# Kernel optimization log

Measured on AMD Instinct MI355X. Metric: run time of the kernel, lower is better.

The kernel has to match this reference:

```python
import jax, jax.numpy as jnp
import numpy as np
import math

E = 1024
H = 16
R = 16
ALPHA = 16
SCALING = ALPHA / R
T, B, S = 2048, 2, 2048


def setup_inputs() -> dict:
    key = jax.random.key(0)
    ks = jax.random.split(key, 20)
    d = {
        "query": jax.random.normal(ks[0], (T, B, E), jnp.float32),
        "key": jax.random.normal(ks[1], (S, B, E), jnp.float32),
        "value": jax.random.normal(ks[2], (S, B, E), jnp.float32),
    }
    i = 3
    for name in ("q", "k", "v", "o"):
        d[name + "_w"] = jax.random.normal(ks[i], (E, E), jnp.float32) * 0.02; i += 1
        d[name + "_b"] = jax.random.normal(ks[i], (E,), jnp.float32) * 0.02; i += 1
        d[name + "_la"] = jax.random.normal(ks[i], (R, E), jnp.float32) * 0.02; i += 1
        d[name + "_lb"] = jax.random.normal(ks[i], (E, R), jnp.float32) * 0.02; i += 1
    return d


def _lora_linear(x, w, b, la, lb):
    # y = x @ w.T + b + scaling * (x @ la.T) @ lb.T
    return x @ w.T + b + SCALING * ((x @ la.T) @ lb.T)


def reference(query, key, value,
              q_w, q_b, q_la, q_lb,
              k_w, k_b, k_la, k_lb,
              v_w, v_b, v_la, v_lb,
              o_w, o_b, o_la, o_lb):
    tgt_len, bsz, embed_dim = query.shape
    src_len = key.shape[0]
    head_dim = embed_dim // H
    q = _lora_linear(query, q_w, q_b, q_la, q_lb)
    k = _lora_linear(key, k_w, k_b, k_la, k_lb)
    v = _lora_linear(value, v_w, v_b, v_la, v_lb)
    # (T, B, E) -> (B*H, T, hd)
    q = q.reshape(tgt_len, bsz * H, head_dim).transpose(1, 0, 2)
    k = k.reshape(src_len, bsz * H, head_dim).transpose(1, 0, 2)
    v = v.reshape(src_len, bsz * H, head_dim).transpose(1, 0, 2)
    scale = 1.0 / math.sqrt(float(head_dim))
    scores = jnp.einsum("btd,bsd->bts", q * scale, k)  # (B*H, T, S)
    attn = jax.nn.softmax(scores, axis=-1)
    out = jnp.einsum("bts,bsd->btd", attn, v)  # (B*H, T, hd)
    out = out.transpose(1, 0, 2).reshape(tgt_len * bsz, embed_dim)
    out = _lora_linear(out, o_w, o_b, o_la, o_lb)
    out = out.reshape(tgt_len, bsz, embed_dim)
    attn_w = attn.reshape(bsz, H, tgt_len, src_len).mean(axis=1)
    return out, attn_w
```

## Files before the change

kernel.cpp:

```cpp
#include <hip/hip_runtime.h>
#include <stdint.h>

#define E_DIM 1024
#define KAUG 1056
#define N_HEADS 16
#define HD 64
#define R_LORA 16
#define T_LEN 2048
#define B_SZ 2
#define S_LEN 2048
#define NROW 4096
#define Q_SCALE 0.1803368801111204f

#define XG_N ((size_t)NROW * KAUG)
#define WG_N ((size_t)E_DIM * KAUG)
#define HSZ  ((size_t)B_SZ * N_HEADS * T_LEN * HD)

typedef unsigned short USH;
typedef __bf16 bf16x8 __attribute__((ext_vector_type(8)));
typedef float  f32x4  __attribute__((ext_vector_type(4)));

__device__ __forceinline__ USH f2bf(float f) {
    uint32_t u = __builtin_bit_cast(uint32_t, f);
    return (USH)((u + 0x7FFFu + ((u >> 16) & 1u)) >> 16);
}
__device__ __forceinline__ float bf2f(USH s) {
    uint32_t u = ((uint32_t)s) << 16;
    return __builtin_bit_cast(float, u);
}
__device__ __forceinline__ void async_cp16(const void* g, void* l) {
    __builtin_amdgcn_global_load_lds(
        (const __attribute__((address_space(1))) void*)g,
        (__attribute__((address_space(3))) void*)l, 16, 0, 0);
}
__device__ __forceinline__ uint32_t pack_bf_trunc(float x, float y) {
    return __builtin_amdgcn_perm(__builtin_bit_cast(uint32_t, y),
                                 __builtin_bit_cast(uint32_t, x), 0x07060302u);
}

__global__ __launch_bounds__(256) void lora_aug_x3_kernel(
    const float* __restrict__ Xq, const float* __restrict__ Xk,
    const float* __restrict__ Xv,
    const float* __restrict__ laq, const float* __restrict__ lak,
    const float* __restrict__ lav, USH* __restrict__ Xg_base) {
    int n = blockIdx.x, y = blockIdx.y, tid = threadIdx.x;
    const float* X  = (y == 0) ? Xq : (y == 1) ? Xk : Xv;
    const float* la = (y == 0) ? laq : (y == 1) ? lak : lav;
    USH* Xg = Xg_base + (size_t)y * XG_N;

    float4 xv = *(const float4*)(X + (size_t)n * E_DIM + tid * 4);
    ushort4 ox;
    ox.x = f2bf(xv.x); ox.y = f2bf(xv.y); ox.z = f2bf(xv.z); ox.w = f2bf(xv.w);
    *(ushort4*)(Xg + (size_t)n * KAUG + tid * 4) = ox;

    float acc[R_LORA];
#pragma unroll
    for (int r = 0; r < R_LORA; ++r) {
        float4 lv = *(const float4*)(la + (size_t)r * E_DIM + tid * 4);
        acc[r] = xv.x * lv.x + xv.y * lv.y + xv.z * lv.z + xv.w * lv.w;
    }
#pragma unroll
    for (int r = 0; r < R_LORA; ++r) {
        float v = acc[r];
#pragma unroll
        for (int off = 32; off > 0; off >>= 1) v += __shfl_down(v, off, 64);
        acc[r] = v;
    }
    __shared__ float red[R_LORA][4];
    int lane = tid & 63, wid = tid >> 6;
    if (lane == 0) {
#pragma unroll
        for (int r = 0; r < R_LORA; ++r) red[r][wid] = acc[r];
    }
    __syncthreads();
    if (tid < 32) {
        float v = 0.0f;
        if (tid < R_LORA) v = red[tid][0] + red[tid][1] + red[tid][2] + red[tid][3];
        else if (tid == R_LORA) v = 1.0f;
        Xg[(size_t)n * KAUG + 1024 + tid] = f2bf(v);
    }
}

__global__ __launch_bounds__(256) void lora_a_bf16_kernel(
    USH* __restrict__ Xg, const float* __restrict__ la) {
    int n = blockIdx.x, tid = threadIdx.x;
    ushort4 xu = *(const ushort4*)(Xg + (size_t)n * KAUG + tid * 4);
    float x0 = bf2f(xu.x), x1 = bf2f(xu.y), x2 = bf2f(xu.z), x3 = bf2f(xu.w);
    float acc[R_LORA];
#pragma unroll
    for (int r = 0; r < R_LORA; ++r) {
        float4 lv = *(const float4*)(la + (size_t)r * E_DIM + tid * 4);
        acc[r] = x0 * lv.x + x1 * lv.y + x2 * lv.z + x3 * lv.w;
    }
#pragma unroll
    for (int r = 0; r < R_LORA; ++r) {
        float v = acc[r];
#pragma unroll
        for (int off = 32; off > 0; off >>= 1) v += __shfl_down(v, off, 64);
        acc[r] = v;
    }
    __shared__ float red[R_LORA][4];
    int lane = tid & 63, wid = tid >> 6;
    if (lane == 0) {
#pragma unroll
        for (int r = 0; r < R_LORA; ++r) red[r][wid] = acc[r];
    }
    __syncthreads();
    if (tid < 32) {
        float v = 0.0f;
        if (tid < R_LORA) v = red[tid][0] + red[tid][1] + red[tid][2] + red[tid][3];
        else if (tid == R_LORA) v = 1.0f;
        Xg[(size_t)n * KAUG + 1024 + tid] = f2bf(v);
    }
}

__global__ __launch_bounds__(256) void aug_w4_kernel(
    const float* __restrict__ Wq, const float* __restrict__ lbq, const float* __restrict__ bq,
    const float* __restrict__ Wk, const float* __restrict__ lbk, const float* __restrict__ bk_,
    const float* __restrict__ Wv, const float* __restrict__ lbv, const float* __restrict__ bv_,
    const float* __restrict__ Wo, const float* __restrict__ lbo, const float* __restrict__ bo,
    USH* __restrict__ Wg_base) {
    int e = blockIdx.x, y = blockIdx.y, tid = threadIdx.x;
    const float* W    = (y == 0) ? Wq : (y == 1) ? Wk : (y == 2) ? Wv : Wo;
    const float* lb   = (y == 0) ? lbq : (y == 1) ? lbk : (y == 2) ? lbv : lbo;
    const float* bias = (y == 0) ? bq : (y == 1) ? bk_ : (y == 2) ? bv_ : bo;
    USH* Wg = Wg_base + (size_t)y * WG_N;

    float4 v = *(const float4*)(W + (size_t)e * E_DIM + tid * 4);
    ushort4 o;
    o.x = f2bf(v.x); o.y = f2bf(v.y); o.z = f2bf(v.z); o.w = f2bf(v.w);
    *(ushort4*)(Wg + (size_t)e * KAUG + tid * 4) = o;
    if (tid < 32) {
        float t = (tid < R_LORA) ? lb[(size_t)e * R_LORA + tid]
                                 : (tid == R_LORA ? bias[e] : 0.0f);
        Wg[(size_t)e * KAUG + 1024 + tid] = f2bf(t);
    }
}

__global__ __launch_bounds__(256) void gemm_qkv_kernel(
    const USH* __restrict__ Xg_base, const USH* __restrict__ Wg_base,
    USH* __restrict__ qkv_base) {
    __shared__ __align__(16) USH As[2][128 * 32];
    __shared__ __align__(16) USH Bs[2][128 * 32];

    int orig = blockIdx.x + (blockIdx.y << 3) + blockIdx.z * 256;
    int v_ = (orig & 7) * 96 + (orig >> 3);
    int e0 = (v_ & 7) * 128, n0 = ((v_ >> 3) & 31) * 128, z = v_ >> 8;

    const USH* Xg = Xg_base + (size_t)z * XG_N;
    const USH* Wg = Wg_base + (size_t)z * WG_N;
    USH* out = qkv_base + (size_t)z * HSZ;
    float scale = (z == 0) ? Q_SCALE : 1.0f;

    int tid = threadIdx.x;
    int wid = tid >> 6, lane = tid & 63, quad = lane >> 4, l16 = lane & 15;
    int wm = wid & 1, wn = wid >> 1;

    int r0 = wid * 16 + (lane >> 2);
    int k8 = (lane & 3) * 8;

    f32x4 acc[4][4];
    const f32x4 fzero = {0.f, 0.f, 0.f, 0.f};
#pragma unroll
    for (int i = 0; i < 4; ++i)
#pragma unroll
        for (int j = 0; j < 4; ++j) acc[i][j] = fzero;

    async_cp16(Xg + (size_t)(n0 + r0) * KAUG + k8,       As[0] + (wid * 16) * 32);
    async_cp16(Xg + (size_t)(n0 + 64 + r0) * KAUG + k8,  As[0] + (64 + wid * 16) * 32);
    async_cp16(Wg + (size_t)(e0 + r0) * KAUG + k8,       Bs[0] + (wid * 16) * 32);
    async_cp16(Wg + (size_t)(e0 + 64 + r0) * KAUG + k8,  Bs[0] + (64 + wid * 16) * 32);
    __syncthreads();

    int cur = 0;
    for (int kt = 0; kt < KAUG; kt += 32, cur ^= 1) {
        if (kt + 32 < KAUG) {
            int kn = kt + 32;
            async_cp16(Xg + (size_t)(n0 + r0) * KAUG + kn + k8,       As[cur ^ 1] + (wid * 16) * 32);
            async_cp16(Xg + (size_t)(n0 + 64 + r0) * KAUG + kn + k8,  As[cur ^ 1] + (64 + wid * 16) * 32);
            async_cp16(Wg + (size_t)(e0 + r0) * KAUG + kn + k8,       Bs[cur ^ 1] + (wid * 16) * 32);
            async_cp16(Wg + (size_t)(e0 + 64 + r0) * KAUG + kn + k8,  Bs[cur ^ 1] + (64 + wid * 16) * 32);
        }

        bf16x8 af[4], bfr[4];
#pragma unroll
        for (int i = 0; i < 4; ++i)
            af[i] = *(const bf16x8*)&As[cur][(wm * 64 + i * 16 + l16) * 32 + quad * 8];
#pragma unroll
        for (int j = 0; j < 4; ++j)
            bfr[j] = *(const bf16x8*)&Bs[cur][(wn * 64 + j * 16 + l16) * 32 + quad * 8];
#pragma unroll
        for (int i = 0; i < 4; ++i)
#pragma unroll
            for (int j = 0; j < 4; ++j)
                acc[i][j] = __builtin_amdgcn_mfma_f32_16x16x32_bf16(
                    af[i], bfr[j], acc[i][j], 0, 0, 0);

        __syncthreads();
    }

#pragma unroll
    for (int i = 0; i < 4; ++i) {
#pragma unroll
        for (int j = 0; j < 4; ++j) {
#pragma unroll
            for (int r = 0; r < 4; ++r) {
                int nr = n0 + wm * 64 + i * 16 + quad * 4 + r;
                int ec = e0 + wn * 64 + j * 16 + l16;
                float v = acc[i][j][r] * scale;
                int b = nr & 1, h = ec >> 6, d = ec & 63;
                if (z != 2) {
                    int t = nr >> 1;
                    out[(((size_t)(b * 16 + h) * T_LEN + t) << 6) + d] = f2bf(v);
                } else {
                    int s = nr >> 1;
                    out[(((size_t)(b * 16 + h) * HD + d) << 11) + s] = f2bf(v);
                }
            }
        }
    }
}

__global__ __launch_bounds__(256) void gemm_o_kernel(
    const USH* __restrict__ Xg, const USH* __restrict__ Wg,
    float* __restrict__ out) {
    __shared__ __align__(16) USH As[2][64 * 32];
    __shared__ __align__(16) USH Bs[2][128 * 32];

    int orig = blockIdx.x + (blockIdx.y << 3);
    int v_ = ((orig & 7) << 6) + (orig >> 3);
    int e0 = (v_ & 7) * 128, n0 = (v_ >> 3) * 64;

    int tid = threadIdx.x;
    int wid = tid >> 6, lane = tid & 63, quad = lane >> 4, l16 = lane & 15;
    int wm = wid & 1, wn = wid >> 1;
    int r0 = wid * 16 + (lane >> 2);
    int k8 = (lane & 3) * 8;

    f32x4 acc[2][4];
    const f32x4 fzero = {0.f, 0.f, 0.f, 0.f};
#pragma unroll
    for (int i = 0; i < 2; ++i)
#pragma unroll
        for (int j = 0; j < 4; ++j) acc[i][j] = fzero;

    async_cp16(Xg + (size_t)(n0 + r0) * KAUG + k8,       As[0] + (wid * 16) * 32);
    async_cp16(Wg + (size_t)(e0 + r0) * KAUG + k8,       Bs[0] + (wid * 16) * 32);
    async_cp16(Wg + (size_t)(e0 + 64 + r0) * KAUG + k8,  Bs[0] + (64 + wid * 16) * 32);
    __syncthreads();

    int cur = 0;
    for (int kt = 0; kt < KAUG; kt += 32, cur ^= 1) {
        if (kt + 32 < KAUG) {
            int kn = kt + 32;
            async_cp16(Xg + (size_t)(n0 + r0) * KAUG + kn + k8,       As[cur ^ 1] + (wid * 16) * 32);
            async_cp16(Wg + (size_t)(e0 + r0) * KAUG + kn + k8,       Bs[cur ^ 1] + (wid * 16) * 32);
            async_cp16(Wg + (size_t)(e0 + 64 + r0) * KAUG + kn + k8,  Bs[cur ^ 1] + (64 + wid * 16) * 32);
        }

        bf16x8 af[2], bfr[4];
#pragma unroll
        for (int i = 0; i < 2; ++i)
            af[i] = *(const bf16x8*)&As[cur][(wm * 32 + i * 16 + l16) * 32 + quad * 8];
#pragma unroll
        for (int j = 0; j < 4; ++j)
            bfr[j] = *(const bf16x8*)&Bs[cur][(wn * 64 + j * 16 + l16) * 32 + quad * 8];
#pragma unroll
        for (int i = 0; i < 2; ++i)
#pragma unroll
            for (int j = 0; j < 4; ++j)
                acc[i][j] = __builtin_amdgcn_mfma_f32_16x16x32_bf16(
                    af[i], bfr[j], acc[i][j], 0, 0, 0);

        __syncthreads();
    }

#pragma unroll
    for (int i = 0; i < 2; ++i)
#pragma unroll
        for (int j = 0; j < 4; ++j)
#pragma unroll
            for (int r = 0; r < 4; ++r) {
                int nr = n0 + wm * 32 + i * 16 + quad * 4 + r;
                int ec = e0 + wn * 64 + j * 16 + l16;
                out[(size_t)nr * E_DIM + ec] = acc[i][j][r];
            }
}

__global__ __launch_bounds__(256, 4) void flash_mfma_kernel(
    const USH* __restrict__ qp, const USH* __restrict__ kp,
    const USH* __restrict__ vpt, USH* __restrict__ ohg,
    float* __restrict__ lbuf) {
    __shared__ __align__(16) USH Pb[4096];
    __shared__ __align__(16) USH Ks[2][4096];
    __shared__ __align__(16) USH Vs[2][4096];

    int orig = blockIdx.x + (blockIdx.y << 5);
    int v_ = ((orig & 7) << 7) + (orig >> 3);
    int t0 = (v_ & 31) * 64, bh = v_ >> 5;

    int tid = threadIdx.x, w = tid >> 6, lane = tid & 63;
    int quad = lane >> 4, l16 = lane & 15;
    int sw = l16 & 7;
    size_t headO = (size_t)bh * (T_LEN * HD);

    bf16x8 bq[2];
    {
        const USH* qrow = qp + headO + (size_t)(t0 + w * 16 + l16) * HD + quad * 8;
        bq[0] = *(const bf16x8*)qrow;
        bq[1] = *(const bf16x8*)(qrow + 32);
    }

#pragma unroll
    for (int half = 0; half < 2; ++half)
        async_cp16(kp + headO + (size_t)(w * 16 + l16) * HD + half * 32 + quad * 8,
                   &Ks[0][w * 1024 + half * 512]);
    __syncthreads();

    float lsum = 0.f;
    const f32x4 fzero = {0.f, 0.f, 0.f, 0.f};
    f32x4 o[4];
#pragma unroll
    for (int jd = 0; jd < 4; ++jd) o[jd] = fzero;

    USH* pb = Pb + w * 1024;

    for (int it = 0; it < S_LEN / 64; ++it) {
        int s0 = it * 64, cur = it & 1;
        if (it + 1 < S_LEN / 64) {
#pragma unroll
            for (int half = 0; half < 2; ++half)
                async_cp16(kp + headO + (size_t)(s0 + 64 + w * 16 + l16) * HD + half * 32 + quad * 8,
                           &Ks[cur ^ 1][w * 1024 + half * 512]);
        }
#pragma unroll
        for (int half = 0; half < 2; ++half)
            async_cp16(vpt + headO + (size_t)(w * 16 + l16) * S_LEN + s0 + half * 32 + quad * 8,
                       &Vs[cur][w * 1024 + half * 512]);

        bf16x8 ak[4][2];
#pragma unroll
        for (int j = 0; j < 4; ++j)
#pragma unroll
            for (int half = 0; half < 2; ++half)
                ak[j][half] = *(const bf16x8*)&Ks[cur][j * 1024 + half * 512 + quad * 128 + l16 * 8];

        f32x4 sc[4];
        __builtin_amdgcn_s_setprio(1);
#pragma unroll
        for (int j = 0; j < 4; ++j) {
            sc[j] = __builtin_amdgcn_mfma_f32_16x16x32_bf16(ak[j][0], bq[0], fzero, 0, 0, 0);
            sc[j] = __builtin_amdgcn_mfma_f32_16x16x32_bf16(ak[j][1], bq[1], sc[j], 0, 0, 0);
        }
        __builtin_amdgcn_s_setprio(0);

        if (it > 0) {
            bf16x8 ap0 = *(const bf16x8*)&pb[l16 * 64 + (quad ^ sw) * 8];
            bf16x8 ap1 = *(const bf16x8*)&pb[l16 * 64 + ((4 + quad) ^ sw) * 8];
            bf16x8 bv[4][2];
#pragma unroll
            for (int jd = 0; jd < 4; ++jd)
#pragma unroll
                for (int half = 0; half < 2; ++half)
                    bv[jd][half] = *(const bf16x8*)&Vs[cur ^ 1][jd * 1024 + half * 512 + quad * 128 + l16 * 8];
#pragma unroll
            for (int jd = 0; jd < 4; ++jd) {
                o[jd] = __builtin_amdgcn_mfma_f32_16x16x32_bf16(ap0, bv[jd][0], o[jd], 0, 0, 0);
                o[jd] = __builtin_amdgcn_mfma_f32_16x16x32_bf16(ap1, bv[jd][1], o[jd], 0, 0, 0);
            }
        }

        float ls = 0.f;
#pragma unroll
        for (int j = 0; j < 4; ++j)
#pragma unroll
            for (int r = 0; r < 4; ++r) {
                float p = __builtin_amdgcn_exp2f(sc[j][r]);
                sc[j][r] = p;
                ls += p;
            }
        lsum += ls;

#pragma unroll
        for (int j = 0; j < 4; ++j) {
            uint2 dv;
            dv.x = pack_bf_trunc(sc[j][0], sc[j][1]);
            dv.y = pack_bf_trunc(sc[j][2], sc[j][3]);
            int g = (j * 2 + (quad >> 1)) ^ sw;
            *(uint2*)&pb[l16 * 64 + g * 8 + (quad & 1) * 4] = dv;
        }

        __syncthreads();
    }

    {
        bf16x8 ap0 = *(const bf16x8*)&pb[l16 * 64 + (quad ^ sw) * 8];
        bf16x8 ap1 = *(const bf16x8*)&pb[l16 * 64 + ((4 + quad) ^ sw) * 8];
        bf16x8 bv[4][2];
#pragma unroll
        for (int jd = 0; jd < 4; ++jd)
#pragma unroll
            for (int half = 0; half < 2; ++half)
                bv[jd][half] = *(const bf16x8*)&Vs[1][jd * 1024 + half * 512 + quad * 128 + l16 * 8];
#pragma unroll
        for (int jd = 0; jd < 4; ++jd) {
            o[jd] = __builtin_amdgcn_mfma_f32_16x16x32_bf16(ap0, bv[jd][0], o[jd], 0, 0, 0);
            o[jd] = __builtin_amdgcn_mfma_f32_16x16x32_bf16(ap1, bv[jd][1], o[jd], 0, 0, 0);
        }
    }

    lsum += __shfl_xor(lsum, 16, 64);
    lsum += __shfl_xor(lsum, 32, 64);
    float rinv = 1.0f / lsum;

    int b = bh >> 4, h = bh & 15;
    float inv[4];
#pragma unroll
    for (int r = 0; r < 4; ++r)
        inv[r] = __shfl(rinv, (lane & 48) | (quad * 4 + r), 64);
#pragma unroll
    for (int jd = 0; jd < 4; ++jd)
#pragma unroll
        for (int r = 0; r < 4; ++r) {
            int t = t0 + w * 16 + quad * 4 + r;
            int n = t * 2 + b, e = h * 64 + jd * 16 + l16;
            ohg[(size_t)n * KAUG + e] = f2bf(o[jd][r] * inv[r]);
        }
    if (quad == 0)
        lbuf[(size_t)bh * T_LEN + t0 + w * 16 + l16] = rinv;
}

__global__ __launch_bounds__(256, 4) void attnw_mfma_kernel(
    const USH* __restrict__ qp, const USH* __restrict__ kp,
    const float* __restrict__ lbuf, float* __restrict__ aw) {
    __shared__ __align__(16) USH Ks[2][4096];

    int orig = blockIdx.x + (blockIdx.y << 5) + (blockIdx.z << 9);
    int v_ = ((orig & 7) << 7) + (orig >> 3);
    int s0 = (v_ & 31) * 64, t0 = ((v_ >> 5) & 15) * 128, b = v_ >> 9;

    int tid = threadIdx.x, w = tid >> 6, lane = tid & 63;
    int quad = lane >> 4, l16 = lane & 15;

    const f32x4 fzero = {0.f, 0.f, 0.f, 0.f};
    f32x4 acc[2][4];
#pragma unroll
    for (int i2 = 0; i2 < 2; ++i2)
#pragma unroll
        for (int j = 0; j < 4; ++j) acc[i2][j] = fzero;

    {
        size_t head0 = (size_t)(b * 16) * (T_LEN * HD);
#pragma unroll
        for (int half = 0; half < 2; ++half)
            async_cp16(kp + head0 + (size_t)(s0 + w * 16 + l16) * HD + half * 32 + quad * 8,
                       &Ks[0][w * 1024 + half * 512]);
    }
    __syncthreads();

    for (int h = 0; h < N_HEADS; ++h) {
        int bh = b * 16 + h;
        size_t head = (size_t)bh * (T_LEN * HD);
        int cur = h & 1;

        if (h + 1 < N_HEADS) {
            size_t headn = head + (size_t)(T_LEN * HD);
#pragma unroll
            for (int half = 0; half < 2; ++half)
                async_cp16(kp + headn + (size_t)(s0 + w * 16 + l16) * HD + half * 32 + quad * 8,
                           &Ks[cur ^ 1][w * 1024 + half * 512]);
        }

        bf16x8 aq[2][2];
#pragma unroll
        for (int i2 = 0; i2 < 2; ++i2) {
            int i = w * 2 + i2;
            const USH* qrow = qp + head + (size_t)(t0 + i * 16 + l16) * HD + quad * 8;
            aq[i2][0] = *(const bf16x8*)qrow;
            aq[i2][1] = *(const bf16x8*)(qrow + 32);
        }

        float il[2][4];
#pragma unroll
        for (int i2 = 0; i2 < 2; ++i2)
#pragma unroll
            for (int r = 0; r < 4; ++r) {
                int t = t0 + w * 32 + i2 * 16 + quad * 4 + r;
                il[i2][r] = lbuf[(size_t)bh * T_LEN + t];
            }

        bf16x8 bk[4][2];
#pragma unroll
        for (int j = 0; j < 4; ++j)
#pragma unroll
            for (int half = 0; half < 2; ++half)
                bk[j][half] = *(const bf16x8*)&Ks[cur][j * 1024 + half * 512 + quad * 128 + l16 * 8];

#pragma unroll
        for (int i2 = 0; i2 < 2; ++i2) {
#pragma unroll
            for (int j = 0; j < 4; ++j) {
                f32x4 s = __builtin_amdgcn_mfma_f32_16x16x32_bf16(aq[i2][0], bk[j][0], fzero, 0, 0, 0);
                s = __builtin_amdgcn_mfma_f32_16x16x32_bf16(aq[i2][1], bk[j][1], s, 0, 0, 0);
#pragma unroll
                for (int r = 0; r < 4; ++r)
                    acc[i2][j][r] += __builtin_amdgcn_exp2f(s[r]) * il[i2][r];
            }
        }

        __syncthreads();
    }

    const float inv_h = 1.0f / (float)N_HEADS;
#pragma unroll
    for (int i2 = 0; i2 < 2; ++i2)
#pragma unroll
        for (int j = 0; j < 4; ++j)
#pragma unroll
            for (int r = 0; r < 4; ++r) {
                int t = t0 + w * 32 + i2 * 16 + quad * 4 + r;
                aw[(size_t)b * T_LEN * S_LEN + (size_t)t * S_LEN + s0 + j * 16 + l16] =
                    acc[i2][j][r] * inv_h;
            }
}

extern "C" void kernel_launch(void* const* d_in, const int* in_sizes, int n_in,
                              void* d_out, int out_size, void* d_ws, size_t ws_size,
                              hipStream_t stream) {
    (void)in_sizes; (void)n_in; (void)out_size; (void)ws_size;

    const float* query = (const float*)d_in[0];
    const float* key_  = (const float*)d_in[1];
    const float* value = (const float*)d_in[2];
    const float* q_w = (const float*)d_in[3],  *q_b = (const float*)d_in[4];
    const float* q_la = (const float*)d_in[5], *q_lb = (const float*)d_in[6];
    const float* k_w = (const float*)d_in[7],  *k_b = (const float*)d_in[8];
    const float* k_la = (const float*)d_in[9], *k_lb = (const float*)d_in[10];
    const float* v_w = (const float*)d_in[11], *v_b = (const float*)d_in[12];
    const float* v_la = (const float*)d_in[13], *v_lb = (const float*)d_in[14];
    const float* o_w = (const float*)d_in[15], *o_b = (const float*)d_in[16];
    const float* o_la = (const float*)d_in[17], *o_lb = (const float*)d_in[18];

    USH* Xg   = (USH*)d_ws;
    USH* Wg   = Xg + 3 * XG_N;
    USH* qkv  = Wg + 4 * WG_N;
    USH* qp   = qkv;
    USH* kp   = qkv + HSZ;
    USH* vpt  = qkv + 2 * HSZ;
    float* lbuf = (float*)(qkv + 3 * HSZ);

    float* out = (float*)d_out;
    float* aw  = out + (size_t)T_LEN * B_SZ * E_DIM;

    dim3 blk(256);

    lora_aug_x3_kernel<<<dim3(NROW, 3), blk, 0, stream>>>(
        query, key_, value, q_la, k_la, v_la, Xg);
    aug_w4_kernel<<<dim3(E_DIM, 4), blk, 0, stream>>>(
        q_w, q_lb, q_b, k_w, k_lb, k_b, v_w, v_lb, v_b, o_w, o_lb, o_b, Wg);
    gemm_qkv_kernel<<<dim3(E_DIM / 128, NROW / 128, 3), blk, 0, stream>>>(Xg, Wg, qkv);

    flash_mfma_kernel<<<dim3(T_LEN / 64, B_SZ * N_HEADS), blk, 0, stream>>>(
        qp, kp, vpt, Xg, lbuf);
    attnw_mfma_kernel<<<dim3(S_LEN / 64, T_LEN / 128, B_SZ), blk, 0, stream>>>(
        qp, kp, lbuf, aw);

    lora_a_bf16_kernel<<<NROW, blk, 0, stream>>>(Xg, o_la);
    gemm_o_kernel<<<dim3(E_DIM / 128, NROW / 64), blk, 0, stream>>>(
        Xg, Wg + 3 * WG_N, out);
}
```

Measured before the change: 389.4 us.

## Rewrite flash attention with 32x32 MFMA and register-resident P via permlane swap

The flash kernel now uses 32x32x16 bf16 MFMA tiles, with each warp handling 32 query rows and blocks covering 128 queries. The probability tile is repacked in registers with permlane32_swap and fed straight into the PV MFMA, so the LDS staging buffer for P and its one-iteration software lag are gone. K and V for the next tile are prefetched together into double buffers. The intent is to cut LDS traffic and instruction count per FLOP and to raise K/V reuse. The cost is higher register pressure (launch bounds lowered to 2) and half as many blocks.

Measured after the change: 377.3 us. 1.03x faster.

```diff
diff --git a/kernel.cpp b/kernel.cpp
--- a/kernel.cpp
+++ b/kernel.cpp
@@ -19,6 +19,9 @@
 typedef unsigned short USH;
 typedef __bf16 bf16x8 __attribute__((ext_vector_type(8)));
 typedef float  f32x4  __attribute__((ext_vector_type(4)));
+typedef float  f32x16 __attribute__((ext_vector_type(16)));
+typedef unsigned int u32x2 __attribute__((ext_vector_type(2)));
+typedef unsigned int u32x4 __attribute__((ext_vector_type(4)));
 
 __device__ __forceinline__ USH f2bf(float f) {
     uint32_t u = __builtin_bit_cast(uint32_t, f);
@@ -287,147 +290,137 @@
             }
 }
 
-__global__ __launch_bounds__(256, 4) void flash_mfma_kernel(
+__global__ __launch_bounds__(256, 2) void flash_mfma_kernel(
     const USH* __restrict__ qp, const USH* __restrict__ kp,
     const USH* __restrict__ vpt, USH* __restrict__ ohg,
     float* __restrict__ lbuf) {
-    __shared__ __align__(16) USH Pb[4096];
     __shared__ __align__(16) USH Ks[2][4096];
     __shared__ __align__(16) USH Vs[2][4096];
 
-    int orig = blockIdx.x + (blockIdx.y << 5);
-    int v_ = ((orig & 7) << 7) + (orig >> 3);
-    int t0 = (v_ & 31) * 64, bh = v_ >> 5;
+    int orig = blockIdx.x + (blockIdx.y << 4);
+    int v_ = ((orig & 7) << 6) + (orig >> 3);
+    int t0 = (v_ & 15) * 128, bh = v_ >> 4;
 
     int tid = threadIdx.x, w = tid >> 6, lane = tid & 63;
-    int quad = lane >> 4, l16 = lane & 15;
-    int sw = l16 & 7;
+    int lo = lane & 31, hi = lane >> 5;
     size_t headO = (size_t)bh * (T_LEN * HD);
-
-    bf16x8 bq[2];
+    int t_base = t0 + w * 32;
+
+    bf16x8 bq[4];
     {
-        const USH* qrow = qp + headO + (size_t)(t0 + w * 16 + l16) * HD + quad * 8;
-        bq[0] = *(const bf16x8*)qrow;
-        bq[1] = *(const bf16x8*)(qrow + 32);
-    }
-
-#pragma unroll
-    for (int half = 0; half < 2; ++half)
-        async_cp16(kp + headO + (size_t)(w * 16 + l16) * HD + half * 32 + quad * 8,
-                   &Ks[0][w * 1024 + half * 512]);
+        const USH* qrow = qp + headO + (size_t)(t_base + lo) * HD + hi * 8;
+#pragma unroll
+        for (int kb = 0; kb < 4; ++kb)
+            bq[kb] = *(const bf16x8*)(qrow + kb * 16);
+    }
+
+#pragma unroll
+    for (int c = 0; c < 2; ++c) {
+        int f = w * 2 + c;
+        async_cp16(kp + headO + (size_t)((f >> 2) * 32 + lo) * HD + (f & 3) * 16 + hi * 8,
+                   &Ks[0][f * 512]);
+        async_cp16(vpt + headO + (size_t)((f >> 2) * 32 + lo) * S_LEN + (f & 3) * 16 + hi * 8,
+                   &Vs[0][f * 512]);
+    }
     __syncthreads();
 
+    const f32x16 z16 = {0,0,0,0,0,0,0,0,0,0,0,0,0,0,0,0};
+    f32x16 o0 = z16, o1 = z16;
     float lsum = 0.f;
-    const f32x4 fzero = {0.f, 0.f, 0.f, 0.f};
-    f32x4 o[4];
-#pragma unroll
-    for (int jd = 0; jd < 4; ++jd) o[jd] = fzero;
-
-    USH* pb = Pb + w * 1024;
 
     for (int it = 0; it < S_LEN / 64; ++it) {
-        int s0 = it * 64, cur = it & 1;
+        int cur = it & 1;
         if (it + 1 < S_LEN / 64) {
-#pragma unroll
-            for (int half = 0; half < 2; ++half)
-                async_cp16(kp + headO + (size_t)(s0 + 64 + w * 16 + l16) * HD + half * 32 + quad * 8,
-                           &Ks[cur ^ 1][w * 1024 + half * 512]);
-        }
-#pragma unroll
-        for (int half = 0; half < 2; ++half)
-            async_cp16(vpt + headO + (size_t)(w * 16 + l16) * S_LEN + s0 + half * 32 + quad * 8,
-                       &Vs[cur][w * 1024 + half * 512]);
-
-        bf16x8 ak[4][2];
-#pragma unroll
-        for (int j = 0; j < 4; ++j)
-#pragma unroll
-            for (int half = 0; half < 2; ++half)
-                ak[j][half] = *(const bf16x8*)&Ks[cur][j * 1024 + half * 512 + quad * 128 + l16 * 8];
-
-        f32x4 sc[4];
+            int sn = (it + 1) * 64;
+#pragma unroll
+            for (int c = 0; c < 2; ++c) {
+                int f = w * 2 + c;
+                async_cp16(kp + headO + (size_t)(sn + (f >> 2) * 32 + lo) * HD + (f & 3) * 16 + hi * 8,
+                           &Ks[cur ^ 1][f * 512]);
+                async_cp16(vpt + headO + (size_t)((f >> 2) * 32 + lo) * S_LEN + sn + (f & 3) * 16 + hi * 8,
+                           &Vs[cur ^ 1][f * 512]);
+            }
+        }
+
+        f32x16 sc0 = z16, sc1 = z16;
         __builtin_amdgcn_s_setprio(1);
 #pragma unroll
-        for (int j = 0; j < 4; ++j) {
-            sc[j] = __builtin_amdgcn_mfma_f32_16x16x32_bf16(ak[j][0], bq[0], fzero, 0, 0, 0);
-            sc[j] = __builtin_amdgcn_mfma_f32_16x16x32_bf16(ak[j][1], bq[1], sc[j], 0, 0, 0);
+        for (int kb = 0; kb < 4; ++kb) {
+            bf16x8 ak0 = *(const bf16x8*)&Ks[cur][(0 * 4 + kb) * 512 + lane * 8];
+            sc0 = __builtin_amdgcn_mfma_f32_32x32x16_bf16(ak0, bq[kb], sc0, 0, 0, 0);
+        }
+#pragma unroll
+        for (int kb = 0; kb < 4; ++kb) {
+            bf16x8 ak1 = *(const bf16x8*)&Ks[cur][(1 * 4 + kb) * 512 + lane * 8];
+            sc1 = __builtin_amdgcn_mfma_f32_32x32x16_bf16(ak1, bq[kb], sc1, 0, 0, 0);
         }
         __builtin_amdgcn_s_setprio(0);
 
-        if (it > 0) {
-            bf16x8 ap0 = *(const bf16x8*)&pb[l16 * 64 + (quad ^ sw) * 8];
-            bf16x8 ap1 = *(const bf16x8*)&pb[l16 * 64 + ((4 + quad) ^ sw) * 8];
-            bf16x8 bv[4][2];
-#pragma unroll
-            for (int jd = 0; jd < 4; ++jd)
-#pragma unroll
-                for (int half = 0; half < 2; ++half)
-                    bv[jd][half] = *(const bf16x8*)&Vs[cur ^ 1][jd * 1024 + half * 512 + quad * 128 + l16 * 8];
-#pragma unroll
-            for (int jd = 0; jd < 4; ++jd) {
-                o[jd] = __builtin_amdgcn_mfma_f32_16x16x32_bf16(ap0, bv[jd][0], o[jd], 0, 0, 0);
-                o[jd] = __builtin_amdgcn_mfma_f32_16x16x32_bf16(ap1, bv[jd][1], o[jd], 0, 0, 0);
-            }
-        }
-
-        float ls = 0.f;
-#pragma unroll
-        for (int j = 0; j < 4; ++j)
-#pragma unroll
-            for (int r = 0; r < 4; ++r) {
-                float p = __builtin_amdgcn_exp2f(sc[j][r]);
-                sc[j][r] = p;
-                ls += p;
-            }
-        lsum += ls;
-
-#pragma unroll
-        for (int j = 0; j < 4; ++j) {
-            uint2 dv;
-            dv.x = pack_bf_trunc(sc[j][0], sc[j][1]);
-            dv.y = pack_bf_trunc(sc[j][2], sc[j][3]);
-            int g = (j * 2 + (quad >> 1)) ^ sw;
-            *(uint2*)&pb[l16 * 64 + g * 8 + (quad & 1) * 4] = dv;
-        }
+        float ls0 = 0.f, ls1 = 0.f, ls2 = 0.f, ls3 = 0.f;
+#pragma unroll
+        for (int r = 0; r < 16; ++r) {
+            float p0 = __builtin_amdgcn_exp2f(sc0[r]);
+            float p1 = __builtin_amdgcn_exp2f(sc1[r]);
+            sc0[r] = p0; sc1[r] = p1;
+            if ((r & 3) == 0)      { ls0 += p0; ls0 += p1; }
+            else if ((r & 3) == 1) { ls1 += p0; ls1 += p1; }
+            else if ((r & 3) == 2) { ls2 += p0; ls2 += p1; }
+            else                   { ls3 += p0; ls3 += p1; }
+        }
+        lsum += (ls0 + ls1) + (ls2 + ls3);
+
+        bf16x8 pa[4];
+#pragma unroll
+        for (int st = 0; st < 2; ++st) {
+#pragma unroll
+            for (int hh = 0; hh < 2; ++hh) {
+                const f32x16& s_ = st ? sc1 : sc0;
+                uint32_t a0 = pack_bf_trunc(s_[hh * 8 + 0], s_[hh * 8 + 1]);
+                uint32_t a1 = pack_bf_trunc(s_[hh * 8 + 2], s_[hh * 8 + 3]);
+                uint32_t a2 = pack_bf_trunc(s_[hh * 8 + 4], s_[hh * 8 + 5]);
+                uint32_t a3 = pack_bf_trunc(s_[hh * 8 + 6], s_[hh * 8 + 7]);
+                u32x2 r02 = __builtin_amdgcn_permlane32_swap(a0, a2, false, false);
+                u32x2 r13 = __builtin_amdgcn_permlane32_swap(a1, a3, false, false);
+                u32x4 pd = {r02[0], r13[0], r02[1], r13[1]};
+                pa[st * 2 + hh] = __builtin_bit_cast(bf16x8, pd);
+            }
+        }
+
+        __builtin_amdgcn_s_setprio(1);
+#pragma unroll
+        for (int ks = 0; ks < 4; ++ks) {
+            bf16x8 bv0 = *(const bf16x8*)&Vs[cur][(0 * 4 + ks) * 512 + lane * 8];
+            o0 = __builtin_amdgcn_mfma_f32_32x32x16_bf16(pa[ks], bv0, o0, 0, 0, 0);
+        }
+#pragma unroll
+        for (int ks = 0; ks < 4; ++ks) {
+            bf16x8 bv1 = *(const bf16x8*)&Vs[cur][(1 * 4 + ks) * 512 + lane * 8];
+            o1 = __builtin_amdgcn_mfma_f32_32x32x16_bf16(pa[ks], bv1, o1, 0, 0, 0);
+        }
+        __builtin_amdgcn_s_setprio(0);
 
         __syncthreads();
     }
 
-    {
-        bf16x8 ap0 = *(const bf16x8*)&pb[l16 * 64 + (quad ^ sw) * 8];
-        bf16x8 ap1 = *(const bf16x8*)&pb[l16 * 64 + ((4 + quad) ^ sw) * 8];
-        bf16x8 bv[4][2];
-#pragma unroll
-        for (int jd = 0; jd < 4; ++jd)
-#pragma unroll
-            for (int half = 0; half < 2; ++half)
-                bv[jd][half] = *(const bf16x8*)&Vs[1][jd * 1024 + half * 512 + quad * 128 + l16 * 8];
-#pragma unroll
-        for (int jd = 0; jd < 4; ++jd) {
-            o[jd] = __builtin_amdgcn_mfma_f32_16x16x32_bf16(ap0, bv[jd][0], o[jd], 0, 0, 0);
-            o[jd] = __builtin_amdgcn_mfma_f32_16x16x32_bf16(ap1, bv[jd][1], o[jd], 0, 0, 0);
-        }
-    }
-
-    lsum += __shfl_xor(lsum, 16, 64);
     lsum += __shfl_xor(lsum, 32, 64);
     float rinv = 1.0f / lsum;
 
     int b = bh >> 4, h = bh & 15;
-    float inv[4];
-#pragma unroll
-    for (int r = 0; r < 4; ++r)
-        inv[r] = __shfl(rinv, (lane & 48) | (quad * 4 + r), 64);
-#pragma unroll
-    for (int jd = 0; jd < 4; ++jd)
-#pragma unroll
-        for (int r = 0; r < 4; ++r) {
-            int t = t0 + w * 16 + quad * 4 + r;
-            int n = t * 2 + b, e = h * 64 + jd * 16 + l16;
-            ohg[(size_t)n * KAUG + e] = f2bf(o[jd][r] * inv[r]);
-        }
-    if (quad == 0)
-        lbuf[(size_t)bh * T_LEN + t0 + w * 16 + l16] = rinv;
+    float inv[16];
+#pragma unroll
+    for (int r = 0; r < 16; ++r) {
+        int rr = (r & 3) + 8 * (r >> 2) + 4 * hi;
+        inv[r] = __shfl(rinv, rr, 64);
+    }
+#pragma unroll
+    for (int r = 0; r < 16; ++r) {
+        int t = t_base + (r & 3) + 8 * (r >> 2) + 4 * hi;
+        size_t nrow = (size_t)(t * 2 + b) * KAUG + h * 64;
+        ohg[nrow + lo]      = f2bf(o0[r] * inv[r]);
+        ohg[nrow + 32 + lo] = f2bf(o1[r] * inv[r]);
+    }
+    if (lane < 32)
+        lbuf[(size_t)bh * T_LEN + t_base + lane] = rinv;
 }
 
 __global__ __launch_bounds__(256, 4) void attnw_mfma_kernel(
@@ -560,7 +553,7 @@
         q_w, q_lb, q_b, k_w, k_lb, k_b, v_w, v_lb, v_b, o_w, o_lb, o_b, Wg);
     gemm_qkv_kernel<<<dim3(E_DIM / 128, NROW / 128, 3), blk, 0, stream>>>(Xg, Wg, qkv);
 
-    flash_mfma_kernel<<<dim3(T_LEN / 64, B_SZ * N_HEADS), blk, 0, stream>>>(
+    flash_mfma_kernel<<<dim3(T_LEN / 128, B_SZ * N_HEADS), blk, 0, stream>>>(
         qp, kp, vpt, Xg, lbuf);
     attnw_mfma_kernel<<<dim3(S_LEN / 64, T_LEN / 128, B_SZ), blk, 0, stream>>>(
         qp, kp, lbuf, aw);
```
